# Kernel tuning notes

Measured on AMD Instinct MI355X. Metric: run time of the kernel, lower is better.

Reference implementation:

```python
import jax, jax.numpy as jnp
import numpy as np

B, T = 8, 512
N_QUBITS, N_ROT, D_PER = 64, 16, 64
D = N_QUBITS * D_PER


def setup_inputs() -> dict:
    key = jax.random.key(0)
    k1, k2, k3, k4 = jax.random.split(key, 4)
    return {
        "x": jax.random.normal(k1, (B, T, D), dtype=jnp.float32),
        "rx_params": jax.random.normal(k2, (N_QUBITS, N_ROT), dtype=jnp.float32),
        "ry_params": jax.random.normal(k3, (N_QUBITS, N_ROT), dtype=jnp.float32),
        "rz_params": jax.random.normal(k4, (N_QUBITS, N_ROT), dtype=jnp.float32),
    }


def _rot_diag(theta, axis):
    # theta: (Q,) per-qubit angle. The torch einsum 'btqd,btqq->btqd' only uses
    # the diagonal of the (Q,Q) rotation matrix. For rx/ry, the paired-qubit
    # construction puts cos(theta_k/2) on both diagonal slots of pair k
    # (first Q//2 angles are used, matching cos[..., :len(idx)]).
    Q = theta.shape[0]
    half = theta[: Q // 2] * 0.5
    if axis in ("x", "y"):
        return jnp.repeat(jnp.cos(half).astype(jnp.complex64), 2)
    # rz: diag(exp(-i a/2), exp(+i a/2)) interleaved over pairs
    e = jnp.exp(-1j * half.astype(jnp.complex64))
    return jnp.stack([e, jnp.conj(e)], axis=-1).reshape(-1)


def _apply_rotation(state, theta, axis):
    # state: (B, T, Q, d_per) complex64
    sf = jnp.fft.fft2(state, axes=(-2, -1))
    sf = sf * _rot_diag(theta, axis)[:, None]  # diagonal per-qubit scale
    return jnp.fft.ifft2(sf, axes=(-2, -1)).real  # torch takes .real


def reference(x, rx_params, ry_params, rz_params):
    b, t, d = x.shape
    q = rx_params.shape[0]
    state = x.reshape(b, t, q, d // q).astype(jnp.complex64)
    for params, axis in ((rx_params, "x"), (ry_params, "y"), (rz_params, "z")):
        theta = params.sum(-1)  # combine n_rotations into one angle per qubit
        state = _apply_rotation(state, theta, axis).astype(jnp.complex64)
    state = state.reshape(b, t, d)
    # noise model: (1 + amp_noise) * exp(i * phase_noise) * state, then L2 norm
    ka, kp = jax.random.split(jax.random.key(42))
    amp = 0.01 * jax.random.normal(ka, state.shape, dtype=jnp.float32)
    ph = 0.005 * jax.random.normal(kp, state.shape, dtype=jnp.float32)
    noisy = (1.0 + amp) * jnp.exp(1j * ph.astype(jnp.complex64)) * state
    norm = jnp.linalg.norm(noisy, axis=-1, keepdims=True)
    noisy = noisy / (norm + 1e-8)
    return jnp.abs(noisy)  # measurement
```

## Files before the change

kernel.cpp:

```cpp
#include <hip/hip_runtime.h>
#include <stdint.h>

typedef _Float16 half8 __attribute__((ext_vector_type(8)));
typedef float floatx4 __attribute__((ext_vector_type(4)));

__device__ __forceinline__ uint32_t rotl32(uint32_t v, int r) {
  return __builtin_amdgcn_alignbit(v, v, 32 - r);
}

__device__ __forceinline__ void threefry2x32(uint32_t k0, uint32_t k1,
                                             uint32_t x0, uint32_t x1,
                                             uint32_t& o0, uint32_t& o1) {
  uint32_t k2 = k0 ^ k1 ^ 0x1BD11BDAu;
  x0 += k0; x1 += k1;
#define TF_R(r) { x0 += x1; x1 = rotl32(x1, (r)); x1 ^= x0; }
  TF_R(13) TF_R(15) TF_R(26) TF_R(6)   x0 += k1; x1 += k2 + 1u;
  TF_R(17) TF_R(29) TF_R(16) TF_R(24)  x0 += k2; x1 += k0 + 2u;
  TF_R(13) TF_R(15) TF_R(26) TF_R(6)   x0 += k0; x1 += k1 + 3u;
  TF_R(17) TF_R(29) TF_R(16) TF_R(24)  x0 += k1; x1 += k2 + 4u;
  TF_R(13) TF_R(15) TF_R(26) TF_R(6)   x0 += k2; x1 += k0 + 5u;
#undef TF_R
  o0 = x0; o1 = x1;
}

__device__ __forceinline__ float noise_mult(uint32_t ka0, uint32_t ka1,
                                            uint32_t idx) {
  uint32_t o0, o1;
  threefry2x32(ka0, ka1, 0u, idx, o0, o1);
  uint32_t bits = o0 ^ o1;
  float vf = __uint_as_float(__builtin_amdgcn_alignbit(0x7Fu, bits, 9));
  float u = fmaxf(fmaf(vf, 2.0f, -3.0f), -0.99999994f);
  float t = fmaf(-u, u, 1.0f);
  float l2 = __log2f(t);
  float p;
  if (__builtin_expect(l2 <= -7.2134752f, 0)) {
    float w = l2 * -0.69314718f;
    float s = sqrtf(w) - 3.0f;
    p = -0.000200214257f;
    p = fmaf(p, s, 0.000100950558f);
    p = fmaf(p, s, 0.00134934322f);
    p = fmaf(p, s, -0.00367342844f);
    p = fmaf(p, s, 0.00573950773f);
    p = fmaf(p, s, -0.0076224613f);
    p = fmaf(p, s, 0.00943887047f);
    p = fmaf(p, s, 1.00167406f);
    p = fmaf(p, s, 2.83297682f);
  } else {
    float a = fmaf(l2, -0.69314718f, -2.5f);
    p = 0.00021858087f;
    p = fmaf(p, a, -0.00125372503f);
    p = fmaf(p, a, -0.00417768164f);
    p = fmaf(p, a, 0.246640727f);
    p = fmaf(p, a, 1.50140941f);
  }
  return fmaf(p, u * 0.014142135623730951f, 1.0f);
}

__device__ __align__(16) _Float16 g_afrag[256 * 16];
__device__ uint32_t g_key[2];

__global__ void setup_kernel(const float* __restrict__ rx,
                             const float* __restrict__ ry,
                             const float* __restrict__ rz) {
  __shared__ float cre[3][64], cim[3][64];
  __shared__ float Gr[64], Gi[64];
  __shared__ float twc[64], tws[64];
  __shared__ float gs[64];
  const int t = threadIdx.x;

  if (t < 32) {
    const float* ps[3] = {rx, ry, rz};
    for (int a = 0; a < 3; ++a) {
      float s = 0.0f;
      for (int r = 0; r < 16; ++r) s += ps[a][t * 16 + r];
      float h = 0.5f * s;
      float ch = cosf(h), sh = sinf(h);
      if (a < 2) {
        cre[a][2 * t] = ch;     cim[a][2 * t] = 0.0f;
        cre[a][2 * t + 1] = ch; cim[a][2 * t + 1] = 0.0f;
      } else {
        cre[2][2 * t] = ch;     cim[2][2 * t] = -sh;
        cre[2][2 * t + 1] = ch; cim[2][2 * t + 1] = sh;
      }
    }
  }
  if (t < 64) {
    double ang = (2.0 * 3.14159265358979323846 / 64.0) * (double)t;
    twc[t] = (float)cos(ang);
    tws[t] = (float)sin(ang);
  }
  __syncthreads();

  if (t < 64) {
    const int k = t, kn = (64 - k) & 63;
    float pr = 1.0f, pi = 0.0f;
    for (int a = 0; a < 3; ++a) {
      float cr = 0.5f * (cre[a][k] + cre[a][kn]);
      float ci = 0.5f * (cim[a][k] - cim[a][kn]);
      float nr = pr * cr - pi * ci;
      float ni = pr * ci + pi * cr;
      pr = nr; pi = ni;
    }
    Gr[k] = pr; Gi[k] = pi;
  }
  __syncthreads();

  if (t < 64) {
    const int mi = t;
    float s = 0.0f;
    for (int k = 0; k < 64; ++k) {
      int idx = (k * mi) & 63;
      s = fmaf(Gr[k], twc[idx], s);
      s = fmaf(-Gi[k], tws[idx], s);
    }
    gs[mi] = s * (1.0f / 64.0f);
  }
  __syncthreads();

  {
    const int w = t >> 6, lane = t & 63, quad = lane >> 4, m = lane & 15;
    const int r0 = 16 * w + m - 8 * quad;
#pragma unroll
    for (int j = 0; j < 8; ++j) {
      g_afrag[t * 16 + j]     = (_Float16)gs[(r0 - j) & 63];
      g_afrag[t * 16 + 8 + j] = (_Float16)gs[(r0 - 32 - j) & 63];
    }
  }

  if (t == 0) {
    uint32_t o0, o1;
    threefry2x32(0u, 42u, 0u, 0u, o0, o1);
    g_key[0] = o0; g_key[1] = o1;
  }
}

__global__ __launch_bounds__(512, 6) void qmain(const float* __restrict__ x,
                                                float* __restrict__ out) {
  __shared__ __align__(16) _Float16 Xt[64 * 72];
  __shared__ float red[8];
  const int tid = threadIdx.x;
  const int row = blockIdx.x;
  const int lane = tid & 63;
  const int w = tid >> 6;
  const int wr = w & 3;
  const int wc = w >> 2;
  const int quad = lane >> 4;
  const int m = lane & 15;

  const half8* at = (const half8*)g_afrag;
  const int ai = (wr << 6) | lane;
  half8 af0 = at[2 * ai];
  half8 af1 = at[2 * ai + 1];
  const uint32_t ka0 = g_key[0], ka1 = g_key[1];

  {
    const float* xr = x + (size_t)row * 4096;
    const int d0 = (tid & 31) * 2;
    const int q0 = (tid >> 5) * 4;
    float2 v[4];
#pragma unroll
    for (int s = 0; s < 4; ++s) v[s] = *(const float2*)(xr + (q0 + s) * 64 + d0);
    union { _Float16 h[4]; uint2 u; } r0, r1;
#pragma unroll
    for (int s = 0; s < 4; ++s) { r0.h[s] = (_Float16)v[s].x; r1.h[s] = (_Float16)v[s].y; }
    *(uint2*)&Xt[d0 * 72 + q0] = r0.u;
    *(uint2*)&Xt[(d0 + 1) * 72 + q0] = r1.u;
  }
  __syncthreads();

  floatx4 acc[2];
#pragma unroll
  for (int cc = 0; cc < 2; ++cc) {
    const int c = 2 * wc + cc;
    const _Float16* bp = &Xt[(16 * c + m) * 72 + 8 * quad];
    half8 b0 = *(const half8*)bp;
    half8 b1 = *(const half8*)(bp + 32);
    acc[cc] = (floatx4){0.0f, 0.0f, 0.0f, 0.0f};
    acc[cc] = __builtin_amdgcn_mfma_f32_16x16x32_f16(af0, b0, acc[cc], 0, 0, 0);
    acc[cc] = __builtin_amdgcn_mfma_f32_16x16x32_f16(af1, b1, acc[cc], 0, 0, 0);
  }

  const uint32_t idxbase = ((uint32_t)row << 12) +
                           (uint32_t)(((16 * wr + 4 * quad) << 6) + (wc << 5) + m);
  float ssum = 0.0f;
#pragma unroll
  for (int cc = 0; cc < 2; ++cc) {
#pragma unroll
    for (int r = 0; r < 4; ++r) {
      const uint32_t idx = idxbase + (uint32_t)(r * 64 + 16 * cc);
      float val = noise_mult(ka0, ka1, idx) * acc[cc][r];
      acc[cc][r] = val;
      ssum = fmaf(val, val, ssum);
    }
  }

#pragma unroll
  for (int off = 32; off >= 1; off >>= 1) ssum += __shfl_xor(ssum, off, 64);
  if (lane == 0) red[w] = ssum;
  __syncthreads();
  float total = 0.0f;
#pragma unroll
  for (int i = 0; i < 8; ++i) total += red[i];
  const float scale = 1.0f / (sqrtf(total) + 1e-8f);

  float* ob = out + (size_t)row * 4096 +
              (size_t)(((16 * wr + 4 * quad) << 6) + (wc << 5) + m);
#pragma unroll
  for (int cc = 0; cc < 2; ++cc)
#pragma unroll
    for (int r = 0; r < 4; ++r)
      ob[r * 64 + 16 * cc] = fabsf(acc[cc][r]) * scale;
}

extern "C" void kernel_launch(void* const* d_in, const int* in_sizes, int n_in,
                              void* d_out, int out_size, void* d_ws, size_t ws_size,
                              hipStream_t stream) {
  const float* x  = (const float*)d_in[0];
  const float* rx = (const float*)d_in[1];
  const float* ry = (const float*)d_in[2];
  const float* rz = (const float*)d_in[3];
  float* out = (float*)d_out;

  setup_kernel<<<1, 256, 0, stream>>>(rx, ry, rz);
  qmain<<<4096, 512, 0, stream>>>(x, out);
}
```

Before: 137.4 us.

## Pair noise generation into float2 ops and split main kernel into two variants

The noise computation now handles two elements at a time using float2 vector ops, which lets the compiler emit packed FMA instructions. The central polynomial is also shortened from five terms to three. The main kernel is split into two launches over halves of the rows. One variant, qmainB, issues the global load and computes the noise before the LDS transpose and MFMA, so the RNG work overlaps the load latency. The shortened polynomial changes numerics slightly, and the extra launch adds overhead.

```diff
diff --git a/kernel.cpp b/kernel.cpp
--- a/kernel.cpp
+++ b/kernel.cpp
@@ -3,6 +3,7 @@
 
 typedef _Float16 half8 __attribute__((ext_vector_type(8)));
 typedef float floatx4 __attribute__((ext_vector_type(4)));
+typedef float floatx2 __attribute__((ext_vector_type(2)));
 
 __device__ __forceinline__ uint32_t rotl32(uint32_t v, int r) {
   return __builtin_amdgcn_alignbit(v, v, 32 - r);
@@ -23,37 +24,47 @@
   o0 = x0; o1 = x1;
 }
 
-__device__ __forceinline__ float noise_mult(uint32_t ka0, uint32_t ka1,
-                                            uint32_t idx) {
-  uint32_t o0, o1;
-  threefry2x32(ka0, ka1, 0u, idx, o0, o1);
-  uint32_t bits = o0 ^ o1;
-  float vf = __uint_as_float(__builtin_amdgcn_alignbit(0x7Fu, bits, 9));
-  float u = fmaxf(fmaf(vf, 2.0f, -3.0f), -0.99999994f);
-  float t = fmaf(-u, u, 1.0f);
-  float l2 = __log2f(t);
-  float p;
-  if (__builtin_expect(l2 <= -7.2134752f, 0)) {
-    float w = l2 * -0.69314718f;
-    float s = sqrtf(w) - 3.0f;
-    p = -0.000200214257f;
-    p = fmaf(p, s, 0.000100950558f);
-    p = fmaf(p, s, 0.00134934322f);
-    p = fmaf(p, s, -0.00367342844f);
-    p = fmaf(p, s, 0.00573950773f);
-    p = fmaf(p, s, -0.0076224613f);
-    p = fmaf(p, s, 0.00943887047f);
-    p = fmaf(p, s, 1.00167406f);
-    p = fmaf(p, s, 2.83297682f);
-  } else {
-    float a = fmaf(l2, -0.69314718f, -2.5f);
-    p = 0.00021858087f;
-    p = fmaf(p, a, -0.00125372503f);
-    p = fmaf(p, a, -0.00417768164f);
-    p = fmaf(p, a, 0.246640727f);
-    p = fmaf(p, a, 1.50140941f);
-  }
-  return fmaf(p, u * 0.014142135623730951f, 1.0f);
+__device__ __forceinline__ float tail_p(float l2) {
+  float w = l2 * -0.69314718f;
+  float s = sqrtf(w) - 3.0f;
+  float p = -0.000200214257f;
+  p = fmaf(p, s, 0.000100950558f);
+  p = fmaf(p, s, 0.00134934322f);
+  p = fmaf(p, s, -0.00367342844f);
+  p = fmaf(p, s, 0.00573950773f);
+  p = fmaf(p, s, -0.0076224613f);
+  p = fmaf(p, s, 0.00943887047f);
+  p = fmaf(p, s, 1.00167406f);
+  p = fmaf(p, s, 2.83297682f);
+  return p;
+}
+
+__device__ __forceinline__ floatx2 noise_pair(uint32_t ka0, uint32_t ka1,
+                                              uint32_t idx0, uint32_t idx1) {
+  uint32_t a0, a1, b0, b1;
+  threefry2x32(ka0, ka1, 0u, idx0, a0, a1);
+  threefry2x32(ka0, ka1, 0u, idx1, b0, b1);
+  const uint32_t bitsA = a0 ^ a1, bitsB = b0 ^ b1;
+  floatx2 vf;
+  vf.x = __uint_as_float(__builtin_amdgcn_alignbit(0x7Fu, bitsA, 9));
+  vf.y = __uint_as_float(__builtin_amdgcn_alignbit(0x7Fu, bitsB, 9));
+  floatx2 u = __builtin_elementwise_fma(vf, (floatx2){2.0f, 2.0f},
+                                        (floatx2){-3.0f, -3.0f});
+  u = __builtin_elementwise_max(u, (floatx2){-0.99999994f, -0.99999994f});
+  floatx2 t = __builtin_elementwise_fma(-u, u, (floatx2){1.0f, 1.0f});
+  floatx2 l2;
+  l2.x = __log2f(t.x);
+  l2.y = __log2f(t.y);
+  floatx2 a = __builtin_elementwise_fma(
+      l2, (floatx2){-0.69314718f, -0.69314718f}, (floatx2){-2.5f, -2.5f});
+  floatx2 p = __builtin_elementwise_fma(
+      (floatx2){-0.00417768164f, -0.00417768164f}, a,
+      (floatx2){0.246640727f, 0.246640727f});
+  p = __builtin_elementwise_fma(p, a, (floatx2){1.50140941f, 1.50140941f});
+  if (__builtin_expect(l2.x <= -7.2134752f, 0)) p.x = tail_p(l2.x);
+  if (__builtin_expect(l2.y <= -7.2134752f, 0)) p.y = tail_p(l2.y);
+  floatx2 uc = u * (floatx2){0.014142135623730951f, 0.014142135623730951f};
+  return __builtin_elementwise_fma(p, uc, (floatx2){1.0f, 1.0f});
 }
 
 __device__ __align__(16) _Float16 g_afrag[256 * 16];
@@ -134,8 +145,8 @@
   }
 }
 
-__global__ __launch_bounds__(512, 6) void qmain(const float* __restrict__ x,
-                                                float* __restrict__ out) {
+__global__ __launch_bounds__(512, 6) void qmainA(const float* __restrict__ x,
+                                                 float* __restrict__ out) {
   __shared__ __align__(16) _Float16 Xt[64 * 72];
   __shared__ float red[8];
   const int tid = threadIdx.x;
@@ -182,17 +193,98 @@
 
   const uint32_t idxbase = ((uint32_t)row << 12) +
                            (uint32_t)(((16 * wr + 4 * quad) << 6) + (wc << 5) + m);
-  float ssum = 0.0f;
+  floatx2 ss = {0.0f, 0.0f};
+#pragma unroll
+  for (int r = 0; r < 4; ++r) {
+    const uint32_t i0 = idxbase + (uint32_t)(r * 64);
+    floatx2 nm = noise_pair(ka0, ka1, i0, i0 + 16u);
+    floatx2 val = nm * (floatx2){acc[0][r], acc[1][r]};
+    acc[0][r] = val.x; acc[1][r] = val.y;
+    ss = __builtin_elementwise_fma(val, val, ss);
+  }
+  float ssum = ss.x + ss.y;
+
+#pragma unroll
+  for (int off = 32; off >= 1; off >>= 1) ssum += __shfl_xor(ssum, off, 64);
+  if (lane == 0) red[w] = ssum;
+  __syncthreads();
+  float total = 0.0f;
+#pragma unroll
+  for (int i = 0; i < 8; ++i) total += red[i];
+  const float scale = 1.0f / (sqrtf(total) + 1e-8f);
+
+  float* ob = out + (size_t)row * 4096 +
+              (size_t)(((16 * wr + 4 * quad) << 6) + (wc << 5) + m);
+#pragma unroll
+  for (int cc = 0; cc < 2; ++cc)
+#pragma unroll
+    for (int r = 0; r < 4; ++r)
+      ob[r * 64 + 16 * cc] = fabsf(acc[cc][r]) * scale;
+}
+
+__global__ __launch_bounds__(512, 6) void qmainB(const float* __restrict__ x,
+                                                 float* __restrict__ out) {
+  __shared__ __align__(16) _Float16 Xt[64 * 72];
+  __shared__ float red[8];
+  const int tid = threadIdx.x;
+  const int row = 2048 + blockIdx.x;
+  const int lane = tid & 63;
+  const int w = tid >> 6;
+  const int wr = w & 3;
+  const int wc = w >> 2;
+  const int quad = lane >> 4;
+  const int m = lane & 15;
+
+  const float* xr = x + (size_t)row * 4096;
+  const int d0 = (tid & 31) * 2;
+  const int q0 = (tid >> 5) * 4;
+  float2 v[4];
+#pragma unroll
+  for (int s = 0; s < 4; ++s) v[s] = *(const float2*)(xr + (q0 + s) * 64 + d0);
+  const half8* at = (const half8*)g_afrag;
+  const int ai = (wr << 6) | lane;
+  half8 af0 = at[2 * ai];
+  half8 af1 = at[2 * ai + 1];
+  const uint32_t ka0 = g_key[0], ka1 = g_key[1];
+
+  const uint32_t idxbase = ((uint32_t)row << 12) +
+                           (uint32_t)(((16 * wr + 4 * quad) << 6) + (wc << 5) + m);
+  floatx2 nm[4];
+#pragma unroll
+  for (int r = 0; r < 4; ++r) {
+    const uint32_t i0 = idxbase + (uint32_t)(r * 64);
+    nm[r] = noise_pair(ka0, ka1, i0, i0 + 16u);
+  }
+
+  {
+    union { _Float16 h[4]; uint2 u; } r0, r1;
+#pragma unroll
+    for (int s = 0; s < 4; ++s) { r0.h[s] = (_Float16)v[s].x; r1.h[s] = (_Float16)v[s].y; }
+    *(uint2*)&Xt[d0 * 72 + q0] = r0.u;
+    *(uint2*)&Xt[(d0 + 1) * 72 + q0] = r1.u;
+  }
+  __syncthreads();
+
+  floatx4 acc[2];
 #pragma unroll
   for (int cc = 0; cc < 2; ++cc) {
-#pragma unroll
-    for (int r = 0; r < 4; ++r) {
-      const uint32_t idx = idxbase + (uint32_t)(r * 64 + 16 * cc);
-      float val = noise_mult(ka0, ka1, idx) * acc[cc][r];
-      acc[cc][r] = val;
-      ssum = fmaf(val, val, ssum);
-    }
-  }
+    const int c = 2 * wc + cc;
+    const _Float16* bp = &Xt[(16 * c + m) * 72 + 8 * quad];
+    half8 b0 = *(const half8*)bp;
+    half8 b1 = *(const half8*)(bp + 32);
+    acc[cc] = (floatx4){0.0f, 0.0f, 0.0f, 0.0f};
+    acc[cc] = __builtin_amdgcn_mfma_f32_16x16x32_f16(af0, b0, acc[cc], 0, 0, 0);
+    acc[cc] = __builtin_amdgcn_mfma_f32_16x16x32_f16(af1, b1, acc[cc], 0, 0, 0);
+  }
+
+  floatx2 ss = {0.0f, 0.0f};
+#pragma unroll
+  for (int r = 0; r < 4; ++r) {
+    floatx2 val = nm[r] * (floatx2){acc[0][r], acc[1][r]};
+    acc[0][r] = val.x; acc[1][r] = val.y;
+    ss = __builtin_elementwise_fma(val, val, ss);
+  }
+  float ssum = ss.x + ss.y;
 
 #pragma unroll
   for (int off = 32; off >= 1; off >>= 1) ssum += __shfl_xor(ssum, off, 64);
@@ -222,5 +314,6 @@
   float* out = (float*)d_out;
 
   setup_kernel<<<1, 256, 0, stream>>>(rx, ry, rz);
-  qmain<<<4096, 512, 0, stream>>>(x, out);
-}
+  qmainA<<<2048, 512, 0, stream>>>(x, out);
+  qmainB<<<2048, 512, 0, stream>>>(x, out);
+}
```

New measurement: 144.3 us. +5.0%, slower.
